# Kernel optimization log

Hardware: AMD Instinct MI355X
Metric: run time of the kernel (lower is better)

The kernel has to match this reference:

```python
import jax, jax.numpy as jnp
import numpy as np

L, H, NH, B, S = 6, 768, 12, 4, 1024
D = H // NH
SCALE = 1.0 / np.sqrt(D)
EPS = 1e-5


def setup_inputs() -> dict:
    key = jax.random.key(0)
    ks = jax.random.split(key, 20)
    std = np.sqrt(2.0 / (5.0 * H)).astype(np.float32)
    w = lambda k, shape: (jax.random.normal(k, shape, jnp.float32) * std)
    x = jax.random.normal(ks[0], (B, S, H), jnp.float32)
    lengths = jnp.array([1024, 896, 768, 640])  # no fully-masked rows
    pad_mask = jnp.arange(S)[None, :] >= lengths[:, None]  # True = padding
    inp = {
        "x": x,
        "pad_mask": pad_mask,
        "Wq": w(ks[1], (L, H, H)), "bq": jnp.zeros((L, H), jnp.float32),
        "Wk": w(ks[2], (L, H, H)), "bk": w(ks[3], (L, H)) * 0.1,
        "Wv": w(ks[4], (L, H, H)), "bv": w(ks[5], (L, H)) * 0.1,
        "Wo": w(ks[6], (L, H, H)), "bo": jnp.zeros((L, H), jnp.float32),
        "ln1_g": jnp.ones((L, H), jnp.float32), "ln1_b": jnp.zeros((L, H), jnp.float32),
        "ln2_g": jnp.ones((L, H), jnp.float32), "ln2_b": jnp.zeros((L, H), jnp.float32),
        "W1": w(ks[7], (L, 8 * H, H)), "b1": jnp.zeros((L, 8 * H), jnp.float32),
        "W2": w(ks[8], (L, H, 4 * H)), "b2": jnp.zeros((L, H), jnp.float32),
        "out_g": jnp.ones((H,), jnp.float32), "out_b": jnp.zeros((H,), jnp.float32),
    }
    return inp


def _ln(x, g, b):
    m = jnp.mean(x, axis=-1, keepdims=True)
    v = jnp.mean(jnp.square(x - m), axis=-1, keepdims=True)
    return (x - m) * jax.lax.rsqrt(v + EPS) * g + b


def _encoder(x, pad_mask, params):
    def layer(x, p):
        (Wq, bq, Wk, bk, Wv, bv, Wo, bo, g1, be1, g2, be2, W1, b1, W2, b2) = p
        Bz, Sl, Hd = x.shape
        xn = _ln(x, g1, be1)
        q = (xn @ Wq.T + bq).reshape(Bz, Sl, NH, D)
        k = (xn @ Wk.T + bk).reshape(Bz, Sl, NH, D)
        v = (xn @ Wv.T + bv).reshape(Bz, Sl, NH, D)
        scores = jnp.einsum('bqhd,bkhd->bhqk', q, k) * SCALE
        scores = jnp.where(pad_mask[:, None, None, :], -jnp.inf, scores)
        probs = jax.nn.softmax(scores, axis=-1)
        av = jnp.einsum('bhqk,bkhd->bqhd', probs, v).reshape(Bz, Sl, Hd)
        x = x + (av @ Wo.T + bo)
        xn = _ln(x, g2, be2)
        h = xn @ W1.T + b1
        u, gate = jnp.split(h, 2, axis=-1)
        x = x + (u * jax.nn.gelu(gate, approximate=False)) @ W2.T + b2
        return x, None

    x, _ = jax.lax.scan(layer, x, params)
    return x


def reference(x, pad_mask, Wq, bq, Wk, bk, Wv, bv, Wo, bo,
              ln1_g, ln1_b, ln2_g, ln2_b, W1, b1, W2, b2, out_g, out_b):
    params = (Wq, bq, Wk, bk, Wv, bv, Wo, bo,
              ln1_g, ln1_b, ln2_g, ln2_b, W1, b1, W2, b2)
    x = _encoder(x, pad_mask, params)
    return _ln(x, out_g, out_b)
```

## Files before the change

kernel.cpp:

```cpp
#include <hip/hip_runtime.h>

typedef unsigned short u16;
typedef __bf16 bf16x8 __attribute__((ext_vector_type(8)));
typedef unsigned short us8 __attribute__((ext_vector_type(8)));
typedef unsigned short us4 __attribute__((ext_vector_type(4)));
typedef float f32x4 __attribute__((ext_vector_type(4)));

typedef __attribute__((address_space(3))) unsigned int as3_uint;
typedef const __attribute__((address_space(1))) unsigned int as1_cuint;

__device__ __forceinline__ u16 f2bf(float f) {
    unsigned u = __float_as_uint(f);
    u += 0x7FFFu + ((u >> 16) & 1u);
    return (u16)(u >> 16);
}
__device__ __forceinline__ float bf2f(u16 h) {
    return __uint_as_float(((unsigned)h) << 16);
}
__device__ __forceinline__ bf16x8 ld8(const u16* p) {
    return __builtin_bit_cast(bf16x8, *(const us8*)p);
}
#define MFMA16(a, b, c) __builtin_amdgcn_mfma_f32_16x16x32_bf16(a, b, c, 0, 0, 0)

__device__ __forceinline__ void glds16(const void* g, void* l) {
    __builtin_amdgcn_global_load_lds((as1_cuint*)g, (as3_uint*)l, 16, 0, 0);
}

__global__ void detect_k(const unsigned* __restrict__ pm, int* __restrict__ len4) {
    __shared__ int isbool;
    const int t = threadIdx.x;
    if (t == 0) isbool = 0;
    __syncthreads();
    unsigned orv = pm[t] | pm[256 + t] | pm[512 + t] | pm[768 + t];
    if (orv & 0xFFFFFF00u) atomicOr(&isbool, 1);
    __syncthreads();
    const int w = t >> 6, l = t & 63;
    int cnt = 0;
    if (isbool) {
        const unsigned char* p8 = (const unsigned char*)pm;
        for (int i = l; i < 1024; i += 64) cnt += (p8[w * 1024 + i] == 0) ? 1 : 0;
    } else {
        for (int i = l; i < 1024; i += 64) cnt += (pm[w * 1024 + i] == 0u) ? 1 : 0;
    }
#pragma unroll
    for (int m = 1; m < 64; m <<= 1) cnt += __shfl_xor(cnt, m);
    if (l == 0) {
        int c = cnt;
        if (c < 1) c = 1;
        if (c > 1024) c = 1024;
        len4[w] = c;
    }
}

__global__ __launch_bounds__(256) void conv_k(
    const float* __restrict__ Wq, const float* __restrict__ Wk,
    const float* __restrict__ Wv, const float* __restrict__ Wo,
    const float* __restrict__ W1, const float* __restrict__ W2,
    const float* __restrict__ bq, const float* __restrict__ bk,
    const float* __restrict__ bv,
    u16* __restrict__ wall, float* __restrict__ bqkv6) {
    const int lyr = blockIdx.y;
    const int idx = blockIdx.x * 256 + threadIdx.x;
    const size_t e = (size_t)idx * 8;
    const float* src;
    if (e < 2359296u) {
        int which = (int)(e / 589824u);
        size_t off = e % 589824u;
        const float* m = (which == 0) ? Wq : (which == 1) ? Wk : (which == 2) ? Wv : Wo;
        src = m + (size_t)lyr * 589824u + off;
    } else if (e < 7077888u) {
        src = W1 + (size_t)lyr * 4718592u + (e - 2359296u);
    } else {
        src = W2 + (size_t)lyr * 2359296u + (e - 7077888u);
    }
    u16* dst = wall + (size_t)lyr * 9437184u + e;
    float4 v0 = ((const float4*)src)[0];
    float4 v1 = ((const float4*)src)[1];
    us8 o;
    o[0] = f2bf(v0.x); o[1] = f2bf(v0.y); o[2] = f2bf(v0.z); o[3] = f2bf(v0.w);
    o[4] = f2bf(v1.x); o[5] = f2bf(v1.y); o[6] = f2bf(v1.z); o[7] = f2bf(v1.w);
    *(us8*)dst = o;
    if (idx < 2304) {
        float bb = (idx < 768) ? bq[lyr * 768 + idx]
                 : (idx < 1536) ? bk[lyr * 768 + idx - 768]
                                : bv[lyr * 768 + idx - 1536];
        bqkv6[lyr * 2304 + idx] = bb;
    }
}

template <int OUTF>
__global__ __launch_bounds__(256) void ln_k(const float* __restrict__ x,
                                            const float* __restrict__ gm,
                                            const float* __restrict__ bt,
                                            void* __restrict__ outp) {
    const int w = threadIdx.x >> 6, l = threadIdx.x & 63;
    const int row = blockIdx.x * 4 + w;
    const float4* xr = (const float4*)(x + (size_t)row * 768);
    float4 v[3];
    float s = 0.f, ss = 0.f;
#pragma unroll
    for (int i = 0; i < 3; ++i) {
        v[i] = xr[i * 64 + l];
        s += v[i].x + v[i].y + v[i].z + v[i].w;
        ss += v[i].x * v[i].x + v[i].y * v[i].y + v[i].z * v[i].z + v[i].w * v[i].w;
    }
#pragma unroll
    for (int m = 1; m < 64; m <<= 1) {
        s += __shfl_xor(s, m);
        ss += __shfl_xor(ss, m);
    }
    const float mean = s * (1.f / 768.f);
    float var = ss * (1.f / 768.f) - mean * mean;
    var = fmaxf(var, 0.f);
    const float rs = rsqrtf(var + 1e-5f);
    const float4* g4 = (const float4*)gm;
    const float4* b4 = (const float4*)bt;
#pragma unroll
    for (int i = 0; i < 3; ++i) {
        float4 gg = g4[i * 64 + l], bb = b4[i * 64 + l];
        float o0 = (v[i].x - mean) * rs * gg.x + bb.x;
        float o1 = (v[i].y - mean) * rs * gg.y + bb.y;
        float o2 = (v[i].z - mean) * rs * gg.z + bb.z;
        float o3 = (v[i].w - mean) * rs * gg.w + bb.w;
        if (OUTF) {
            ((float4*)outp)[(size_t)row * 192 + i * 64 + l] = make_float4(o0, o1, o2, o3);
        } else {
            us4 pk;
            pk[0] = f2bf(o0); pk[1] = f2bf(o1); pk[2] = f2bf(o2); pk[3] = f2bf(o3);
            ((us4*)outp)[(size_t)row * 192 + i * 64 + l] = pk;
        }
    }
}

template <int VAR, int NF, int CHAIN, int PRO>
__device__ __forceinline__ void g256_body(
    const u16* __restrict__ Ab, const u16* __restrict__ Bb0,
    const u16* __restrict__ Bb1,
    const u16* __restrict__ AbN, const u16* __restrict__ Bb0N,
    const u16* __restrict__ Bb1N,
    const float* __restrict__ bias, u16* __restrict__ outp,
    u16* __restrict__ vT, int ldout, int ncol0, int m0,
    u16 (&lds)[2][4][8192]) {
    const int tid = threadIdx.x;
    const int w = tid >> 6, l = tid & 63, ax = l & 15, gx = l >> 4;
    const int wr = w >> 2, wc = w & 3;
    const int K = 768;

    const int row0 = tid >> 2, cc0 = (tid & 3) ^ ((row0 >> 1) & 3);
    const int row1 = 128 + row0, cc1 = (tid & 3) ^ ((row1 >> 1) & 3);
    const size_t goA0 = (size_t)row0 * K + cc0 * 8;
    const size_t goA1 = (size_t)row1 * K + cc1 * 8;

    auto stage = [&](int u, int kt, int nxt) {
        const int kh = u & 1;
        const size_t koff = (size_t)kt * 64 + kh * 32;
        u16* d = (u16*)&lds[kt & 1][u][0];
        const u16* A_ = nxt ? AbN : Ab;
        const u16* B0_ = nxt ? Bb0N : Bb0;
        const u16* B1_ = nxt ? Bb1N : Bb1;
        if (u < 2) {
            glds16(A_ + goA0 + koff, d + tid * 8);
            glds16(A_ + goA1 + koff, d + (512 + tid) * 8);
        } else {
            glds16(B0_ + goA0 + koff, d + tid * 8);
            glds16(B1_ + goA1 + koff, d + (512 + tid) * 8);
        }
    };

    bf16x8 rav[4], rbv[NF];
    f32x4 acc[8][NF] = {};

    auto phase = [&](int buf, int q, int kh, int readB, int vm, int su, int skt,
                     int nxt) {
        if (vm == 8) asm volatile("s_waitcnt vmcnt(8)" ::: "memory");
        else if (vm == 4) asm volatile("s_waitcnt vmcnt(4)" ::: "memory");
        else if (vm == 0) asm volatile("s_waitcnt vmcnt(0)" ::: "memory");
        __builtin_amdgcn_s_barrier();
        if (readB) {
#pragma unroll
            for (int j = 0; j < NF; ++j) {
                int row;
                if (VAR == 0) row = wc * (16 * NF) + j * 16 + ax;
                else row = ((j >= NF / 2) ? 128 : 0) + wc * (8 * NF) +
                           (j % (NF / 2)) * 16 + ax;
                rbv[j] = ld8(&lds[buf][2 + kh][row * 32 + ((gx ^ ((row >> 1) & 3)) * 8)]);
            }
        }
#pragma unroll
        for (int mf = 0; mf < 4; ++mf) {
            int row = wr * 128 + q * 64 + mf * 16 + ax;
            rav[mf] = ld8(&lds[buf][kh][row * 32 + ((gx ^ ((row >> 1) & 3)) * 8)]);
        }
        if (su >= 0) stage(su, skt, nxt);
        asm volatile("s_waitcnt lgkmcnt(0)" ::: "memory");
        __builtin_amdgcn_sched_barrier(0);
        __builtin_amdgcn_s_setprio(1);
#pragma unroll
        for (int mf = 0; mf < 4; ++mf)
#pragma unroll
            for (int j = 0; j < NF; ++j)
                acc[q * 4 + mf][j] = MFMA16(rav[mf], rbv[j], acc[q * 4 + mf][j]);
        __builtin_amdgcn_s_setprio(0);
    };

    if (PRO) {
        stage(0, 0, 0); stage(2, 0, 0); stage(1, 0, 0);
        stage(3, 0, 0); stage(0, 1, 0); stage(2, 1, 0);
    }

#pragma unroll 1
    for (int t = 0; t < 5; ++t) {
        const int O = 2 * t + 1, E2 = 2 * t + 2, O2 = 2 * t + 3;
        phase(0, 0, 0, 1, 8, 1, O, 0);
        phase(0, 1, 0, 0, -1, 3, O, 0);
        phase(0, 0, 1, 1, 8, 0, E2, 0);
        phase(0, 1, 1, 0, -1, 2, E2, 0);
        phase(1, 0, 0, 1, 8, 1, E2, 0);
        phase(1, 1, 0, 0, -1, 3, E2, 0);
        phase(1, 0, 1, 1, 8, 0, O2, 0);
        phase(1, 1, 1, 0, -1, 2, O2, 0);
    }
    if (CHAIN) {
        phase(0, 0, 0, 1, 8, 1, 11, 0);
        phase(0, 1, 0, 0, -1, 3, 11, 0);
        phase(0, 0, 1, 1, 8, 0, 0, 1);
        phase(0, 1, 1, 0, -1, 2, 0, 1);
        phase(1, 0, 0, 1, 8, 1, 0, 1);
        phase(1, 1, 0, 0, -1, 3, 0, 1);
        phase(1, 0, 1, 1, 8, 0, 1, 1);
        phase(1, 1, 1, 0, -1, 2, 1, 1);
    } else {
        phase(0, 0, 0, 1, 8, 1, 11, 0);
        phase(0, 1, 0, 0, -1, 3, 11, 0);
        phase(0, 0, 1, 1, 8, -1, 0, 0);
        phase(0, 1, 1, 0, -1, -1, 0, 0);
        phase(1, 0, 0, 1, 4, -1, 0, 0);
        phase(1, 1, 0, 0, -1, -1, 0, 0);
        phase(1, 0, 1, 1, 0, -1, 0, 0);
        phase(1, 1, 1, 0, -1, -1, 0, 0);
    }

    const int rowb = m0 + wr * 128;
    if (VAR == 0) {
        if (ncol0 >= 1536) {
#pragma unroll
            for (int j = 0; j < NF; ++j) {
                const int col = ncol0 + wc * (16 * NF) + j * 16 + ax;
                const float bn = bias[col];
                u16* vcol = vT + (size_t)(col - 1536) * 4096;
#pragma unroll
                for (int am = 0; am < 8; ++am) {
                    const int rb_ = rowb + am * 16 + 4 * gx;
                    us4 pk;
#pragma unroll
                    for (int r = 0; r < 4; ++r) pk[r] = f2bf(acc[am][j][r] + bn);
                    *(us4*)(vcol + rb_) = pk;
                }
            }
        } else {
#pragma unroll
            for (int j = 0; j < NF; ++j) {
                const int col = ncol0 + wc * (16 * NF) + j * 16 + ax;
                const float bn = bias[col];
#pragma unroll
                for (int am = 0; am < 8; ++am) {
                    const int rb_ = rowb + am * 16 + 4 * gx;
#pragma unroll
                    for (int r = 0; r < 4; ++r)
                        outp[(size_t)(rb_ + r) * ldout + col] = f2bf(acc[am][j][r] + bn);
                }
            }
        }
    } else {
        const int P = NF / 2;
#pragma unroll
        for (int nf = 0; nf < NF / 2; ++nf) {
            const int col = ncol0 + wc * (16 * P) + nf * 16 + ax;
            const float bu_ = bias[col], bg_ = bias[3072 + col];
#pragma unroll
            for (int am = 0; am < 8; ++am) {
                const int rb_ = rowb + am * 16 + 4 * gx;
#pragma unroll
                for (int r = 0; r < 4; ++r) {
                    float uu = acc[am][nf][r] + bu_;
                    float gg = acc[am][P + nf][r] + bg_;
                    float gel = 0.5f * gg * (1.f + erff(gg * 0.70710678118f));
                    outp[(size_t)(rb_ + r) * ldout + col] = f2bf(uu * gel);
                }
            }
        }
    }
}

__global__ __launch_bounds__(512, 2) void qkv256_k(
    const u16* __restrict__ A, const u16* __restrict__ W,
    const float* __restrict__ bias, u16* __restrict__ outp,
    u16* __restrict__ vT) {
    __shared__ __align__(16) u16 lds[2][4][8192];
    const int bid = blockIdx.x;
    const int swz = (bid & 7) * 24 + (bid >> 3);
    const int nb = swz >> 4, mb = swz & 15;
    const int m0 = mb * 256;
    const u16* Ab = A + (size_t)m0 * 768;
    const u16* Bb0 = W + (size_t)(nb * 192) * 768;
    g256_body<0, 3, 0, 1>(Ab, Bb0, Bb0, nullptr, nullptr, nullptr,
                          bias, outp, vT, 2304, nb * 192, m0, lds);
}

__global__ __launch_bounds__(512, 2) void ffn1_k(
    const u16* __restrict__ A, const u16* __restrict__ W,
    const float* __restrict__ bias, u16* __restrict__ outp) {
    __shared__ __align__(16) u16 lds[2][4][8192];
    const int bid = blockIdx.x;
    const int swz = (bid & 7) * 32 + (bid >> 3);
    const int nb = swz >> 4, mb = swz & 15;
    const int m0 = mb * 256;
    const u16* Ab = A + (size_t)m0 * 768;
    const u16* Bb0 = W + (size_t)(nb * 128) * 768;
    const u16* Bb1 = W + (size_t)(3072 + nb * 128 - 128) * 768;
    const u16* Bb0h = W + (size_t)(2048 + nb * 64) * 768;
    const u16* Bb1h = W + (size_t)(5120 + nb * 64 - 128) * 768;
    g256_body<1, 4, 1, 1>(Ab, Bb0, Bb1, Ab, Bb0h, Bb1h,
                          bias, outp, nullptr, 3072, nb * 128, m0, lds);
    g256_body<1, 2, 0, 0>(Ab, Bb0h, Bb1h, nullptr, nullptr, nullptr,
                          bias, outp, nullptr, 3072, 2048 + nb * 64, m0, lds);
}

template <int EPI>
__global__ __launch_bounds__(512) void gemm_k(
    const u16* __restrict__ A, const u16* __restrict__ W,
    const float* __restrict__ bias, const float* __restrict__ resid,
    void* __restrict__ outp, int N, int K) {
    __shared__ __align__(16) u16 smem[2 * 8192 + 2 * 6144];
    const int tid = threadIdx.x;
    const int w = tid >> 6, l = tid & 63, a = l & 15, g = l >> 4;
    const int wr = w >> 2, wc = (w >> 1) & 1, kz = w & 1;
    const int m0 = blockIdx.y * 128, n0 = blockIdx.x * 96;
    f32x4 acc[4][3] = {};
    const int nk = K >> 6;

    auto stage = [&](int kt, int buf) {
        const int k0 = kt * 64;
        u16* dA = smem + buf * 8192;
        u16* dB = smem + 16384 + buf * 6144;
#pragma unroll
        for (int i = 0; i < 2; ++i) {
            int c = i * 512 + tid;
            int row = c >> 3, cc = c & 7, c8 = cc ^ (row & 7);
            glds16(A + (size_t)(m0 + row) * K + k0 + c8 * 8, dA + c * 8);
        }
        {
            int c = tid;
            int row = c >> 3, cc = c & 7, c8 = cc ^ (row & 7);
            glds16(W + (size_t)(n0 + row) * K + k0 + c8 * 8, dB + c * 8);
        }
        {
            int c = 512 + (tid & 255);
            int row = c >> 3, cc = c & 7, c8 = cc ^ (row & 7);
            glds16(W + (size_t)(n0 + row) * K + k0 + c8 * 8, dB + c * 8);
        }
    };

    stage(0, 0);
    int cur = 0;
    for (int kt = 0; kt < nk; ++kt) {
        if (kt + 1 < nk) {
            stage(kt + 1, cur ^ 1);
            __builtin_amdgcn_sched_barrier(0);
            asm volatile("s_waitcnt vmcnt(4)" ::: "memory");
        } else {
            __builtin_amdgcn_sched_barrier(0);
            asm volatile("s_waitcnt vmcnt(0)" ::: "memory");
        }
        __builtin_amdgcn_s_barrier();
        const u16* dA = smem + cur * 8192;
        const u16* dB = smem + 16384 + cur * 6144;
        bf16x8 af[4], bv_[3];
#pragma unroll
        for (int m = 0; m < 4; ++m) {
            int row = wr * 64 + m * 16 + a;
            af[m] = ld8(&dA[row * 64 + (((kz * 4 + g) ^ (a & 7)) * 8)]);
        }
#pragma unroll
        for (int n = 0; n < 3; ++n) {
            int row = wc * 48 + n * 16 + a;
            bv_[n] = ld8(&dB[row * 64 + (((kz * 4 + g) ^ (a & 7)) * 8)]);
        }
        asm volatile("s_waitcnt lgkmcnt(0)" ::: "memory");
        __builtin_amdgcn_sched_barrier(0);
        __builtin_amdgcn_s_setprio(1);
#pragma unroll
        for (int m = 0; m < 4; ++m)
#pragma unroll
            for (int n = 0; n < 3; ++n)
                acc[m][n] = MFMA16(af[m], bv_[n], acc[m][n]);
        __builtin_amdgcn_s_setprio(0);
        __builtin_amdgcn_s_barrier();
        cur ^= 1;
    }

    __syncthreads();
    float* sc = (float*)smem;
    const int quad = wr * 2 + wc;
    if (kz == 1) {
#pragma unroll
        for (int m = 0; m < 4; ++m)
#pragma unroll
            for (int n = 0; n < 3; ++n)
#pragma unroll
                for (int r = 0; r < 4; ++r)
                    sc[quad * 3136 + (m * 16 + 4 * g + r) * 49 + n * 16 + a] =
                        acc[m][n][r];
    }
    __syncthreads();
    if (kz == 0) {
        u16* outu = (u16*)outp;
        float* outf = (float*)outp;
        const int row0 = m0 + wr * 64, col0 = n0 + wc * 48;
#pragma unroll
        for (int n = 0; n < 3; ++n) {
            const int col = col0 + n * 16 + a;
            const float bn = bias[col];
#pragma unroll
            for (int m = 0; m < 4; ++m) {
                const int rb = row0 + m * 16 + 4 * g;
#pragma unroll
                for (int r = 0; r < 4; ++r) {
                    const size_t off = (size_t)(rb + r) * N + col;
                    float vv = acc[m][n][r] + bn +
                               sc[quad * 3136 + (m * 16 + 4 * g + r) * 49 + n * 16 + a];
                    if constexpr (EPI == 0) {
                        outu[off] = f2bf(vv);
                    } else {
                        outf[off] = vv + resid[off];
                    }
                }
            }
        }
    }
}

__global__ __launch_bounds__(256) void attn_k(const u16* __restrict__ qkv,
                                              const u16* __restrict__ vT,
                                              u16* __restrict__ av,
                                              const int* __restrict__ len4) {
    __shared__ __align__(16) u16 Ks[64 * 64];
    __shared__ __align__(16) u16 Vt[64 * 64];
    __shared__ __align__(16) u16 Ps[4][16 * 64];
    const int tid = threadIdx.x;
    const int w = tid >> 6, l = tid & 63, a = l & 15, g = l >> 4;
    const int qb = blockIdx.x, h = blockIdx.y, b = blockIdx.z;
    const size_t rowQ = (size_t)(b * 1024 + qb * 64 + w * 16 + a);
    const u16* qp = qkv + rowQ * 2304 + h * 64;
    bf16x8 qf[2];
    qf[0] = __builtin_bit_cast(bf16x8, *(const us8*)(qp + g * 8));
    qf[1] = __builtin_bit_cast(bf16x8, *(const us8*)(qp + 32 + g * 8));
    f32x4 O[4] = {};
    float m_r[4], l_r[4];
#pragma unroll
    for (int r = 0; r < 4; ++r) { m_r[r] = -1e30f; l_r[r] = 0.f; }
    const int length = len4[b];
    const int nkt = (length + 63) >> 6;
    for (int kt = 0; kt < nkt; ++kt) {
        __syncthreads();
#pragma unroll
        for (int i = 0; i < 2; ++i) {
            int c = i * 256 + tid;
            int row = c >> 3, cc = c & 7, c8 = cc ^ (row & 7);
            glds16(qkv + (size_t)(b * 1024 + kt * 64 + row) * 2304 + 768 + h * 64 + c8 * 8,
                   &Ks[c * 8]);
        }
        {
            const int d = l;
            const u16* vrow = vT + (size_t)(h * 64 + d) * 4096 + b * 1024 + kt * 64;
#pragma unroll
            for (int i = 0; i < 2; ++i) {
                int kkc = w + 4 * i;
                us8 vv = *(const us8*)(vrow + kkc * 8);
                int cc = kkc ^ (d & 7);
                *(us8*)&Vt[d * 64 + cc * 8] = vv;
            }
        }
        __syncthreads();
        f32x4 s[4] = {};
#pragma unroll
        for (int ks = 0; ks < 2; ++ks) {
#pragma unroll
            for (int f = 0; f < 4; ++f) {
                int row = f * 16 + a;
                bf16x8 kf = ld8(&Ks[row * 64 + (((ks * 4 + g) ^ (a & 7)) * 8)]);
                s[f] = MFMA16(qf[ks], kf, s[f]);
            }
        }
        float mloc[4] = {-1e30f, -1e30f, -1e30f, -1e30f};
#pragma unroll
        for (int f = 0; f < 4; ++f) {
            int kkg = kt * 64 + f * 16 + a;
            bool valid = kkg < length;
#pragma unroll
            for (int r = 0; r < 4; ++r) {
                float v = valid ? s[f][r] * 0.125f : -1e30f;
                s[f][r] = v;
                mloc[r] = fmaxf(mloc[r], v);
            }
        }
#pragma unroll
        for (int r = 0; r < 4; ++r) {
#pragma unroll
            for (int m = 1; m < 16; m <<= 1)
                mloc[r] = fmaxf(mloc[r], __shfl_xor(mloc[r], m));
        }
        float al[4], ps[4];
#pragma unroll
        for (int r = 0; r < 4; ++r) {
            float nm = fmaxf(m_r[r], mloc[r]);
            al[r] = __expf(m_r[r] - nm);
            m_r[r] = nm;
            ps[r] = 0.f;
        }
#pragma unroll
        for (int f = 0; f < 4; ++f)
#pragma unroll
            for (int r = 0; r < 4; ++r) {
                float p = __expf(s[f][r] - m_r[r]);
                s[f][r] = p;
                ps[r] += p;
            }
#pragma unroll
        for (int r = 0; r < 4; ++r) {
#pragma unroll
            for (int m = 1; m < 16; m <<= 1) ps[r] += __shfl_xor(ps[r], m);
            l_r[r] = l_r[r] * al[r] + ps[r];
        }
#pragma unroll
        for (int df = 0; df < 4; ++df)
#pragma unroll
            for (int r = 0; r < 4; ++r) O[df][r] *= al[r];
#pragma unroll
        for (int f = 0; f < 4; ++f)
#pragma unroll
            for (int r = 0; r < 4; ++r) {
                int prow = 4 * g + r;
                int cc = (2 * f + (a >> 3)) ^ (prow & 7);
                Ps[w][prow * 64 + cc * 8 + (a & 7)] = f2bf(s[f][r]);
            }
        asm volatile("s_waitcnt lgkmcnt(0)" ::: "memory");
        __builtin_amdgcn_sched_barrier(0);
#pragma unroll
        for (int ks = 0; ks < 2; ++ks) {
            bf16x8 pf = ld8(&Ps[w][a * 64 + (((ks * 4 + g) ^ (a & 7)) * 8)]);
#pragma unroll
            for (int df = 0; df < 4; ++df) {
                int vrow = df * 16 + a;
                bf16x8 vf = ld8(&Vt[vrow * 64 + (((ks * 4 + g) ^ (a & 7)) * 8)]);
                O[df] = MFMA16(pf, vf, O[df]);
            }
        }
    }
#pragma unroll
    for (int df = 0; df < 4; ++df) {
        int col = h * 64 + df * 16 + a;
#pragma unroll
        for (int r = 0; r < 4; ++r) {
            int row = b * 1024 + qb * 64 + w * 16 + 4 * g + r;
            av[(size_t)row * 768 + col] = f2bf(O[df][r] / l_r[r]);
        }
    }
}

extern "C" void kernel_launch(void* const* d_in, const int* in_sizes, int n_in,
                              void* d_out, int out_size, void* d_ws, size_t ws_size,
                              hipStream_t stream) {
    const float* x_in = (const float*)d_in[0];
    const unsigned* pm = (const unsigned*)d_in[1];
    const float* Wq = (const float*)d_in[2];
    const float* bq = (const float*)d_in[3];
    const float* Wk = (const float*)d_in[4];
    const float* bk = (const float*)d_in[5];
    const float* Wv = (const float*)d_in[6];
    const float* bv = (const float*)d_in[7];
    const float* Wo = (const float*)d_in[8];
    const float* bo = (const float*)d_in[9];
    const float* g1 = (const float*)d_in[10];
    const float* be1 = (const float*)d_in[11];
    const float* g2 = (const float*)d_in[12];
    const float* be2 = (const float*)d_in[13];
    const float* W1 = (const float*)d_in[14];
    const float* b1 = (const float*)d_in[15];
    const float* W2 = (const float*)d_in[16];
    const float* b2 = (const float*)d_in[17];
    const float* og = (const float*)d_in[18];
    const float* ob = (const float*)d_in[19];

    char* ws = (char*)d_ws;
    u16* wall  = (u16*)(ws + 0);
    float* bqkv6 = (float*)(ws + 113246208);
    int* len4  = (int*)(ws + 113301504);
    float* xbuf = (float*)(ws + 113301760);
    u16* xn    = (u16*)(ws + 125884672);
    u16* qkv   = (u16*)(ws + 132176128);
    u16* avb   = (u16*)(ws + 151050496);
    u16* ub    = (u16*)(ws + 157341952);
    u16* vT    = (u16*)(ws + 157341952);

    detect_k<<<1, 256, 0, stream>>>(pm, len4);
    conv_k<<<dim3(4608, 6), 256, 0, stream>>>(Wq, Wk, Wv, Wo, W1, W2, bq, bk, bv,
                                              wall, bqkv6);
    for (int l = 0; l < 6; ++l) {
        u16* wl = wall + (size_t)l * 9437184u;
        const float* xcur = (l == 0) ? x_in : xbuf;
        ln_k<0><<<1024, 256, 0, stream>>>(xcur, g1 + l * 768, be1 + l * 768, xn);
        qkv256_k<<<192, 512, 0, stream>>>(xn, wl, bqkv6 + l * 2304, qkv, vT);
        attn_k<<<dim3(16, 12, 4), 256, 0, stream>>>(qkv, vT, avb, len4);
        gemm_k<1><<<dim3(8, 32), 512, 0, stream>>>(avb, wl + 3 * 589824, bo + l * 768,
                                                   xcur, xbuf, 768, 768);
        ln_k<0><<<1024, 256, 0, stream>>>(xbuf, g2 + l * 768, be2 + l * 768, xn);
        ffn1_k<<<256, 512, 0, stream>>>(xn, wl + 2359296, b1 + l * 6144, ub);
        gemm_k<1><<<dim3(8, 32), 512, 0, stream>>>(ub, wl + 7077888, b2 + l * 768, xbuf,
                                                   xbuf, 768, 3072);
    }
    ln_k<1><<<1024, 256, 0, stream>>>(xbuf, og, ob, d_out);
}
```

Measured before the change: 1.185 ms.

## Double-buffer K/V tiles in attention and halve per-thread width in weight conversion

The attention kernel now keeps two LDS buffers for K and V tiles. It issues the next tile's async K copy and V global loads before computing on the current tile, then writes V into LDS after the softmax work, so global latency overlaps compute and one barrier per iteration is removed. Separately, the weight conversion kernel now has each thread convert 4 floats instead of 8, with twice as many blocks launched. The changes add LDS use and register pressure, and the conversion change alters the memory access granularity.

```diff
diff --git a/kernel.cpp b/kernel.cpp
--- a/kernel.cpp
+++ b/kernel.cpp
@@ -61,7 +61,7 @@
     u16* __restrict__ wall, float* __restrict__ bqkv6) {
     const int lyr = blockIdx.y;
     const int idx = blockIdx.x * 256 + threadIdx.x;
-    const size_t e = (size_t)idx * 8;
+    const size_t e = (size_t)idx * 4;
     const float* src;
     if (e < 2359296u) {
         int which = (int)(e / 589824u);
@@ -74,12 +74,10 @@
         src = W2 + (size_t)lyr * 2359296u + (e - 7077888u);
     }
     u16* dst = wall + (size_t)lyr * 9437184u + e;
-    float4 v0 = ((const float4*)src)[0];
-    float4 v1 = ((const float4*)src)[1];
-    us8 o;
-    o[0] = f2bf(v0.x); o[1] = f2bf(v0.y); o[2] = f2bf(v0.z); o[3] = f2bf(v0.w);
-    o[4] = f2bf(v1.x); o[5] = f2bf(v1.y); o[6] = f2bf(v1.z); o[7] = f2bf(v1.w);
-    *(us8*)dst = o;
+    float4 v = *(const float4*)src;
+    us4 o;
+    o[0] = f2bf(v.x); o[1] = f2bf(v.y); o[2] = f2bf(v.z); o[3] = f2bf(v.w);
+    *(us4*)dst = o;
     if (idx < 2304) {
         float bb = (idx < 768) ? bq[lyr * 768 + idx]
                  : (idx < 1536) ? bk[lyr * 768 + idx - 768]
@@ -444,8 +442,8 @@
                                               const u16* __restrict__ vT,
                                               u16* __restrict__ av,
                                               const int* __restrict__ len4) {
-    __shared__ __align__(16) u16 Ks[64 * 64];
-    __shared__ __align__(16) u16 Vt[64 * 64];
+    __shared__ __align__(16) u16 Ks[2][64 * 64];
+    __shared__ __align__(16) u16 Vt[2][64 * 64];
     __shared__ __align__(16) u16 Ps[4][16 * 64];
     const int tid = threadIdx.x;
     const int w = tid >> 6, l = tid & 63, a = l & 15, g = l >> 4;
@@ -461,34 +459,47 @@
     for (int r = 0; r < 4; ++r) { m_r[r] = -1e30f; l_r[r] = 0.f; }
     const int length = len4[b];
     const int nkt = (length + 63) >> 6;
-    for (int kt = 0; kt < nkt; ++kt) {
-        __syncthreads();
+
+    auto stageK = [&](int kt, int buf) {
 #pragma unroll
         for (int i = 0; i < 2; ++i) {
             int c = i * 256 + tid;
             int row = c >> 3, cc = c & 7, c8 = cc ^ (row & 7);
             glds16(qkv + (size_t)(b * 1024 + kt * 64 + row) * 2304 + 768 + h * 64 + c8 * 8,
-                   &Ks[c * 8]);
-        }
-        {
-            const int d = l;
-            const u16* vrow = vT + (size_t)(h * 64 + d) * 4096 + b * 1024 + kt * 64;
-#pragma unroll
-            for (int i = 0; i < 2; ++i) {
-                int kkc = w + 4 * i;
-                us8 vv = *(const us8*)(vrow + kkc * 8);
-                int cc = kkc ^ (d & 7);
-                *(us8*)&Vt[d * 64 + cc * 8] = vv;
-            }
-        }
-        __syncthreads();
+                   &Ks[buf][c * 8]);
+        }
+    };
+    us8 vv[2];
+    auto loadV = [&](int kt) {
+        const u16* vrow = vT + (size_t)(h * 64 + l) * 4096 + b * 1024 + kt * 64;
+#pragma unroll
+        for (int i = 0; i < 2; ++i) vv[i] = *(const us8*)(vrow + (w + 4 * i) * 8);
+    };
+    auto writeV = [&](int buf) {
+#pragma unroll
+        for (int i = 0; i < 2; ++i) {
+            int kkc = w + 4 * i;
+            int cc = kkc ^ (l & 7);
+            *(us8*)&Vt[buf][l * 64 + cc * 8] = vv[i];
+        }
+    };
+
+    stageK(0, 0);
+    loadV(0);
+    asm volatile("s_waitcnt vmcnt(0)" ::: "memory");
+    writeV(0);
+    __syncthreads();
+    int buf = 0;
+    for (int kt = 0; kt < nkt; ++kt) {
+        const bool pf = (kt + 1 < nkt);
+        if (pf) { stageK(kt + 1, buf ^ 1); loadV(kt + 1); }
         f32x4 s[4] = {};
 #pragma unroll
         for (int ks = 0; ks < 2; ++ks) {
 #pragma unroll
             for (int f = 0; f < 4; ++f) {
                 int row = f * 16 + a;
-                bf16x8 kf = ld8(&Ks[row * 64 + (((ks * 4 + g) ^ (a & 7)) * 8)]);
+                bf16x8 kf = ld8(&Ks[buf][row * 64 + (((ks * 4 + g) ^ (a & 7)) * 8)]);
                 s[f] = MFMA16(qf[ks], kf, s[f]);
             }
         }
@@ -536,6 +547,10 @@
         for (int df = 0; df < 4; ++df)
 #pragma unroll
             for (int r = 0; r < 4; ++r) O[df][r] *= al[r];
+        if (pf) {
+            asm volatile("s_waitcnt vmcnt(0)" ::: "memory");
+            writeV(buf ^ 1);
+        }
 #pragma unroll
         for (int f = 0; f < 4; ++f)
 #pragma unroll
@@ -548,14 +563,16 @@
         __builtin_amdgcn_sched_barrier(0);
 #pragma unroll
         for (int ks = 0; ks < 2; ++ks) {
-            bf16x8 pf = ld8(&Ps[w][a * 64 + (((ks * 4 + g) ^ (a & 7)) * 8)]);
+            bf16x8 pf_ = ld8(&Ps[w][a * 64 + (((ks * 4 + g) ^ (a & 7)) * 8)]);
 #pragma unroll
             for (int df = 0; df < 4; ++df) {
                 int vrow = df * 16 + a;
-                bf16x8 vf = ld8(&Vt[vrow * 64 + (((ks * 4 + g) ^ (a & 7)) * 8)]);
-                O[df] = MFMA16(pf, vf, O[df]);
-            }
-        }
+                bf16x8 vf = ld8(&Vt[buf][vrow * 64 + (((ks * 4 + g) ^ (a & 7)) * 8)]);
+                O[df] = MFMA16(pf_, vf, O[df]);
+            }
+        }
+        __syncthreads();
+        buf ^= 1;
     }
 #pragma unroll
     for (int df = 0; df < 4; ++df) {
@@ -604,7 +621,7 @@
     u16* vT    = (u16*)(ws + 157341952);
 
     detect_k<<<1, 256, 0, stream>>>(pm, len4);
-    conv_k<<<dim3(4608, 6), 256, 0, stream>>>(Wq, Wk, Wv, Wo, W1, W2, bq, bk, bv,
+    conv_k<<<dim3(9216, 6), 256, 0, stream>>>(Wq, Wk, Wv, Wo, W1, W2, bq, bk, bv,
                                               wall, bqkv6);
     for (int l = 0; l < 6; ++l) {
         u16* wl = wall + (size_t)l * 9437184u;
```

Result: no change. 1.180 ms (-0.4%).
